# Kernel optimization log

Hardware: AMD Instinct MI355X
Metric: run time of the kernel (lower is better)

The kernel has to match this reference:

```python
import jax, jax.numpy as jnp
import numpy as np

N_NODES = 100000
N_EDGES = 1600000
IN_DIM, HIDDEN, OUT = 128, 64, 32


def setup_inputs() -> dict:
    key = jax.random.key(0)
    k1, k2, k3, k4 = jax.random.split(key, 4)
    x = jax.random.normal(k1, (N_NODES, IN_DIM), dtype=jnp.float32)
    edge_index = jax.random.randint(k2, (2, N_EDGES), 0, N_NODES, dtype=jnp.int64)
    # Glorot-style init for GCN weights
    W1 = jax.random.normal(k3, (IN_DIM, HIDDEN), dtype=jnp.float32) / np.sqrt(IN_DIM)
    b1 = jnp.zeros((HIDDEN,), dtype=jnp.float32)
    W2 = jax.random.normal(k4, (HIDDEN, OUT), dtype=jnp.float32) / np.sqrt(HIDDEN)
    b2 = jnp.zeros((OUT,), dtype=jnp.float32)
    return {"x": x, "edge_index": edge_index, "W1": W1, "b1": b1, "W2": W2, "b2": b2}


def _gcn_conv(x, src, dst, W, b, n_nodes):
    """PyG GCNConv: h = W x; symmetric-normalized scatter-add over edges
    (self-loops already appended to src/dst)."""
    h = x @ W  # [N, F_out] — transform first (F_out <= F_in)
    ones = jnp.ones_like(dst, dtype=h.dtype)
    deg = jax.ops.segment_sum(ones, dst, num_segments=n_nodes)  # in-degree incl. self-loop
    dinv = jnp.where(deg > 0, jax.lax.rsqrt(deg), 0.0)
    norm = dinv[src] * dinv[dst]  # [E]
    msg = h[src] * norm[:, None]  # [E, F_out] — dominant gather
    agg = jax.ops.segment_sum(msg, dst, num_segments=n_nodes)  # [N, F_out]
    return agg + b


def reference(x, edge_index, W1, b1, W2, b2):
    n_nodes = x.shape[0]
    loops = jnp.arange(n_nodes, dtype=edge_index.dtype)
    src = jnp.concatenate([edge_index[0], loops])
    dst = jnp.concatenate([edge_index[1], loops])
    h = jax.nn.relu(_gcn_conv(x, src, dst, W1, b1, n_nodes))
    out = jax.nn.relu(_gcn_conv(h, src, dst, W2, b2, n_nodes))
    return out
```

## Files before the change

kernel.cpp:

```cpp
#include <hip/hip_runtime.h>

#define IN_DIM 128
#define HID    64
#define OUTD   32

#define BSHIFT 9
#define BNODES 512
#define NB     196
#define BCAP   16384
#define CHUNK  4096

#define XPAD   136

typedef __attribute__((ext_vector_type(8))) short bf16x8;
typedef __attribute__((ext_vector_type(4))) float f32x4;


__device__ __forceinline__ unsigned bfp2(float x, float y) {
    unsigned a = __float_as_uint(x); a = a + 0x7FFF + ((a >> 16) & 1);
    unsigned b = __float_as_uint(y); b = b + 0x7FFF + ((b >> 16) & 1);
    return (a >> 16) | (b & 0xFFFF0000u);
}

__device__ __forceinline__ unsigned short bf1(float x) {
    unsigned u = __float_as_uint(x);
    u += 0x7FFF + ((u >> 16) & 1);
    return (unsigned short)(u >> 16);
}

__device__ __forceinline__ void acc8(float* f, uint4 q) {
    f[0] += __uint_as_float(q.x << 16); f[1] += __uint_as_float(q.x & 0xFFFF0000u);
    f[2] += __uint_as_float(q.y << 16); f[3] += __uint_as_float(q.y & 0xFFFF0000u);
    f[4] += __uint_as_float(q.z << 16); f[5] += __uint_as_float(q.z & 0xFFFF0000u);
    f[6] += __uint_as_float(q.w << 16); f[7] += __uint_as_float(q.w & 0xFFFF0000u);
}


__global__ void k_binit(int* __restrict__ bucketCursor) {
    int t = threadIdx.x;
    if (t < NB) bucketCursor[t] = t * BCAP;
}


__launch_bounds__(256)
__global__ void k_bscatter(const int* __restrict__ src, const int* __restrict__ dst,
                           int* __restrict__ bucketCursor, int* __restrict__ ebuf, int E) {
    __shared__ int h[NB];
    __shared__ int lbase[NB];
    __shared__ int lcur[NB];
    int t = threadIdx.x;
    int base = blockIdx.x * CHUNK;
    int end = min(base + CHUNK, E);
    for (int i = t; i < NB; i += 256) { h[i] = 0; lcur[i] = 0; }
    __syncthreads();
    for (int i = base + t; i < end; i += 256)
        atomicAdd(&h[dst[i] >> BSHIFT], 1);
    __syncthreads();
    for (int i = t; i < NB; i += 256)
        lbase[i] = h[i] ? atomicAdd(&bucketCursor[i], h[i]) : 0;
    __syncthreads();
    for (int i = base + t; i < end; i += 256) {
        int d = dst[i];
        int b = d >> BSHIFT;
        int off = atomicAdd(&lcur[b], 1);
        ebuf[lbase[b] + off] = (src[i] << BSHIFT) | (d & (BNODES - 1));
    }
}


__launch_bounds__(256)
__global__ void k_bfinal(const int* __restrict__ ebuf, const int* __restrict__ bucketCursor,
                         int* __restrict__ rs, int* __restrict__ re, float* __restrict__ dinv,
                         int* __restrict__ csr, int N) {
    __shared__ int hist[BNODES];
    __shared__ int rsl[BNODES];
    __shared__ int ssum[256];
    int t = threadIdx.x;
    int b = blockIdx.x;
    int nodeBase = b << BSHIFT;
    int ebase = b * BCAP;
    int eend = bucketCursor[b];

    hist[t] = 0; hist[t + 256] = 0;
    __syncthreads();
    for (int i = ebase + t; i < eend; i += 256)
        atomicAdd(&hist[__builtin_nontemporal_load(ebuf + i) & (BNODES - 1)], 1);
    __syncthreads();

    int h0 = hist[2 * t], h1 = hist[2 * t + 1];
    ssum[t] = h0 + h1;
    __syncthreads();
    for (int off = 1; off < 256; off <<= 1) {
        int u = (t >= off) ? ssum[t - off] : 0;
        __syncthreads();
        ssum[t] += u;
        __syncthreads();
    }
    int excl = ssum[t] - h0 - h1;
    rsl[2 * t]     = excl;
    rsl[2 * t + 1] = excl + h0;

    int n0 = nodeBase + 2 * t, n1 = n0 + 1;
    if (n0 < N) {
        rs[n0] = ebase + excl;           re[n0] = ebase + excl + h0;
        dinv[n0] = rsqrtf((float)h0 + 1.0f);
    }
    if (n1 < N) {
        rs[n1] = ebase + excl + h0;      re[n1] = ebase + excl + h0 + h1;
        dinv[n1] = rsqrtf((float)h1 + 1.0f);
    }

    hist[2 * t] = 0; hist[2 * t + 1] = 0;
    __syncthreads();

    for (int i = ebase + t; i < eend; i += 256) {
        int p = ebuf[i];
        int l = p & (BNODES - 1);
        int off = atomicAdd(&hist[l], 1);
        csr[ebase + rsl[l] + off] = ((unsigned)p) >> BSHIFT;
    }
}


__launch_bounds__(256)
__global__ void k_gemm1(const float* __restrict__ x, const float* __restrict__ W1,
                        const float* __restrict__ dinv, unsigned short* __restrict__ hs1b, int N) {
    __shared__ unsigned short xsb[64 * XPAD];
    __shared__ unsigned short wsb[64 * XPAD];
    const int t = threadIdx.x;
    const int base = blockIdx.x * 64;

    for (int i = t; i < IN_DIM * HID; i += 256) {
        int k = i >> 6, n = i & 63;
        wsb[n * XPAD + k] = bf1(W1[i]);
    }
    {
        const float4* s4 = (const float4*)(x + (size_t)base * IN_DIM);
        #pragma unroll
        for (int j = 0; j < 8; ++j) {
            int idx = t + j * 256;
            int r = idx >> 5, k4 = (idx & 31) * 4;
            ushort4 o;
            if (base + r < N) {
                float4 v = s4[idx];
                o.x = bf1(v.x); o.y = bf1(v.y); o.z = bf1(v.z); o.w = bf1(v.w);
            } else {
                o.x = 0; o.y = 0; o.z = 0; o.w = 0;
            }
            *(ushort4*)&xsb[r * XPAD + k4] = o;
        }
    }
    __syncthreads();

    const int lane = t & 63;
    const int w    = t >> 6;
    const int lr   = lane & 15;
    const int kg   = lane >> 4;

    f32x4 acc0 = {0,0,0,0}, acc1 = {0,0,0,0}, acc2 = {0,0,0,0}, acc3 = {0,0,0,0};
    #pragma unroll
    for (int kb = 0; kb < 4; ++kb) {
        int ko = kb * 32 + kg * 8;
        bf16x8 af = *(const bf16x8*)&xsb[(w * 16 + lr) * XPAD + ko];
        bf16x8 b0 = *(const bf16x8*)&wsb[( 0 + lr) * XPAD + ko];
        bf16x8 b1 = *(const bf16x8*)&wsb[(16 + lr) * XPAD + ko];
        bf16x8 b2 = *(const bf16x8*)&wsb[(32 + lr) * XPAD + ko];
        bf16x8 b3 = *(const bf16x8*)&wsb[(48 + lr) * XPAD + ko];
        acc0 = __builtin_amdgcn_mfma_f32_16x16x32_bf16(af, b0, acc0, 0, 0, 0);
        acc1 = __builtin_amdgcn_mfma_f32_16x16x32_bf16(af, b1, acc1, 0, 0, 0);
        acc2 = __builtin_amdgcn_mfma_f32_16x16x32_bf16(af, b2, acc2, 0, 0, 0);
        acc3 = __builtin_amdgcn_mfma_f32_16x16x32_bf16(af, b3, acc3, 0, 0, 0);
    }

    #pragma unroll
    for (int j = 0; j < 4; ++j) {
        int node = base + w * 16 + kg * 4 + j;
        if (node < N) {
            float d = dinv[node];
            unsigned short* o = hs1b + (size_t)node * HID + lr;
            o[0]  = bf1(acc0[j] * d);
            o[16] = bf1(acc1[j] * d);
            o[32] = bf1(acc2[j] * d);
            o[48] = bf1(acc3[j] * d);
        }
    }
}


__launch_bounds__(256)
__global__ void k_fuse2(const uint4* __restrict__ hs, const int* __restrict__ rs,
                        const int* __restrict__ re, const int* __restrict__ csr,
                        const float* __restrict__ dinv,
                        const float* __restrict__ b1, const float* __restrict__ W2,
                        uint2* __restrict__ hs2b, int N) {
    __shared__ float Ws[HID * OUTD];
    __shared__ float L1s[32 * 68];
    const int t = threadIdx.x;
    const int base = blockIdx.x * 32;

    for (int i = t; i < HID * OUTD / 4; i += 256)
        ((float4*)Ws)[i] = ((const float4*)W2)[i];

    {
        int node = base + (t >> 3);
        int lane = t & 7;
        float fa[8] = {0,0,0,0,0,0,0,0};
        float fb[8] = {0,0,0,0,0,0,0,0};
        float fc[8] = {0,0,0,0,0,0,0,0};
        float fd[8] = {0,0,0,0,0,0,0,0};
        if (node < N) {
            acc8(fa, hs[(size_t)node * 8 + lane]);
            int i = rs[node], end = re[node];
            for (; i + 4 <= end; i += 4) {
                int s0 = __builtin_nontemporal_load(csr + i);
                int s1 = __builtin_nontemporal_load(csr + i + 1);
                int s2 = __builtin_nontemporal_load(csr + i + 2);
                int s3 = __builtin_nontemporal_load(csr + i + 3);
                uint4 q0 = hs[(size_t)s0 * 8 + lane];
                uint4 q1 = hs[(size_t)s1 * 8 + lane];
                uint4 q2 = hs[(size_t)s2 * 8 + lane];
                uint4 q3 = hs[(size_t)s3 * 8 + lane];
                acc8(fa, q0); acc8(fb, q1); acc8(fc, q2); acc8(fd, q3);
            }
            if (i + 2 <= end) {
                int s0 = __builtin_nontemporal_load(csr + i);
                int s1 = __builtin_nontemporal_load(csr + i + 1);
                uint4 q0 = hs[(size_t)s0 * 8 + lane];
                uint4 q1 = hs[(size_t)s1 * 8 + lane];
                acc8(fa, q0); acc8(fb, q1);
                i += 2;
            }
            if (i < end) {
                int s0 = __builtin_nontemporal_load(csr + i);
                acc8(fa, hs[(size_t)s0 * 8 + lane]);
            }
            float dn = dinv[node];
            const float4* bb4 = (const float4*)(b1 + lane * 8);
            float4 bv0 = bb4[0], bv1 = bb4[1];
            float* Lrow = &L1s[(t >> 3) * 68 + lane * 8];
            Lrow[0] = fmaxf((fa[0] + fb[0] + fc[0] + fd[0]) * dn + bv0.x, 0.0f);
            Lrow[1] = fmaxf((fa[1] + fb[1] + fc[1] + fd[1]) * dn + bv0.y, 0.0f);
            Lrow[2] = fmaxf((fa[2] + fb[2] + fc[2] + fd[2]) * dn + bv0.z, 0.0f);
            Lrow[3] = fmaxf((fa[3] + fb[3] + fc[3] + fd[3]) * dn + bv0.w, 0.0f);
            Lrow[4] = fmaxf((fa[4] + fb[4] + fc[4] + fd[4]) * dn + bv1.x, 0.0f);
            Lrow[5] = fmaxf((fa[5] + fb[5] + fc[5] + fd[5]) * dn + bv1.y, 0.0f);
            Lrow[6] = fmaxf((fa[6] + fb[6] + fc[6] + fd[6]) * dn + bv1.z, 0.0f);
            Lrow[7] = fmaxf((fa[7] + fb[7] + fc[7] + fd[7]) * dn + bv1.w, 0.0f);
        } else {
            float* Lrow = &L1s[(t >> 3) * 68 + lane * 8];
            #pragma unroll
            for (int j = 0; j < 8; ++j) Lrow[j] = 0.0f;
        }
    }
    __syncthreads();

    {
        const int fq = t & 7;
        const int nl = t >> 3;
        float4 a = {0,0,0,0};
        #pragma unroll 8
        for (int k = 0; k < HID; ++k) {
            float4 w = ((const float4*)Ws)[k * 8 + fq];
            float xv = L1s[nl * 68 + k];
            a.x += xv * w.x; a.y += xv * w.y; a.z += xv * w.z; a.w += xv * w.w;
        }
        int n = base + nl;
        if (n < N) {
            float d = dinv[n];
            a.x *= d; a.y *= d; a.z *= d; a.w *= d;
            hs2b[(size_t)n * 8 + fq] = make_uint2(bfp2(a.x, a.y), bfp2(a.z, a.w));
        }
    }
}


__launch_bounds__(256)
__global__ void k_agg2(const uint4* __restrict__ hs, const int* __restrict__ rs,
                       const int* __restrict__ re, const int* __restrict__ csr,
                       const float* __restrict__ dinv,
                       const float* __restrict__ b2, float* __restrict__ out, int N) {
    int tid = blockIdx.x * 256 + threadIdx.x;
    int node = tid >> 2;
    if (node >= N) return;
    int lane = tid & 3;

    float fa[8] = {0,0,0,0,0,0,0,0};
    float fb[8] = {0,0,0,0,0,0,0,0};
    float fc[8] = {0,0,0,0,0,0,0,0};
    float fd[8] = {0,0,0,0,0,0,0,0};
    acc8(fa, hs[(size_t)node * 4 + lane]);
    int i = rs[node], end = re[node];
    for (; i + 4 <= end; i += 4) {
        int s0 = __builtin_nontemporal_load(csr + i);
        int s1 = __builtin_nontemporal_load(csr + i + 1);
        int s2 = __builtin_nontemporal_load(csr + i + 2);
        int s3 = __builtin_nontemporal_load(csr + i + 3);
        uint4 q0 = hs[(size_t)s0 * 4 + lane];
        uint4 q1 = hs[(size_t)s1 * 4 + lane];
        uint4 q2 = hs[(size_t)s2 * 4 + lane];
        uint4 q3 = hs[(size_t)s3 * 4 + lane];
        acc8(fa, q0); acc8(fb, q1); acc8(fc, q2); acc8(fd, q3);
    }
    if (i + 2 <= end) {
        int s0 = __builtin_nontemporal_load(csr + i);
        int s1 = __builtin_nontemporal_load(csr + i + 1);
        uint4 q0 = hs[(size_t)s0 * 4 + lane];
        uint4 q1 = hs[(size_t)s1 * 4 + lane];
        acc8(fa, q0); acc8(fb, q1);
        i += 2;
    }
    if (i < end) {
        int s0 = __builtin_nontemporal_load(csr + i);
        acc8(fa, hs[(size_t)s0 * 4 + lane]);
    }
    float dn = dinv[node];
    const float4* bb4 = (const float4*)(b2 + lane * 8);
    float4 b0 = bb4[0], b1v = bb4[1];
    float4 o0, o1;
    o0.x = fmaxf((fa[0] + fb[0] + fc[0] + fd[0]) * dn + b0.x, 0.0f);
    o0.y = fmaxf((fa[1] + fb[1] + fc[1] + fd[1]) * dn + b0.y, 0.0f);
    o0.z = fmaxf((fa[2] + fb[2] + fc[2] + fd[2]) * dn + b0.z, 0.0f);
    o0.w = fmaxf((fa[3] + fb[3] + fc[3] + fd[3]) * dn + b0.w, 0.0f);
    o1.x = fmaxf((fa[4] + fb[4] + fc[4] + fd[4]) * dn + b1v.x, 0.0f);
    o1.y = fmaxf((fa[5] + fb[5] + fc[5] + fd[5]) * dn + b1v.y, 0.0f);
    o1.z = fmaxf((fa[6] + fb[6] + fc[6] + fd[6]) * dn + b1v.z, 0.0f);
    o1.w = fmaxf((fa[7] + fb[7] + fc[7] + fd[7]) * dn + b1v.w, 0.0f);
    float4* o = (float4*)(out + (size_t)node * OUTD + lane * 8);
    o[0] = o0;
    o[1] = o1;
}


extern "C" void kernel_launch(void* const* d_in, const int* in_sizes, int n_in,
                              void* d_out, int out_size, void* d_ws, size_t ws_size,
                              hipStream_t stream) {
    const float* x  = (const float*)d_in[0];
    const int*   ei = (const int*)  d_in[1];
    const float* W1 = (const float*)d_in[2];
    const float* b1 = (const float*)d_in[3];
    const float* W2 = (const float*)d_in[4];
    const float* b2 = (const float*)d_in[5];

    const int N = in_sizes[0] / IN_DIM;
    const int E = in_sizes[1] / 2;
    const int* srcI = ei;
    const int* dstI = ei + E;
    float* out = (float*)d_out;

    float* dinv         = (float*)d_ws;
    int*   rs           = (int*)d_ws + 131072;
    int*   re           = (int*)d_ws + 2 * 131072;
    int*   bucketCursor = (int*)d_ws + 3 * 131072;
    int*   ebuf         = (int*)d_ws + 4 * 131072;
    int*   csr          = ebuf + (size_t)NB * BCAP;
    uint2* hs1b         = (uint2*)(csr + (size_t)NB * BCAP);
    uint2* hs2b         = hs1b + (size_t)N * 16;

    k_binit   <<<1, 256, 0, stream>>>(bucketCursor);
    k_bscatter<<<(E + CHUNK - 1) / CHUNK, 256, 0, stream>>>(srcI, dstI, bucketCursor, ebuf, E);
    k_bfinal  <<<NB, 256, 0, stream>>>(ebuf, bucketCursor, rs, re, dinv, csr, N);

    k_gemm1<<<(N + 63) / 64, 256, 0, stream>>>(x, W1, dinv, (unsigned short*)hs1b, N);
    k_fuse2<<<(N + 31) / 32, 256, 0, stream>>>((const uint4*)hs1b, rs, re, csr, dinv, b1, W2, hs2b, N);
    k_agg2 <<<(N * 4 + 255) / 256, 256, 0, stream>>>((const uint4*)hs2b, rs, re, csr, dinv, b2, out, N);
}
```

Before: 145.7 us.

## Vectorize edge loads in bucketing kernels and software-pipeline CSR index loads in aggregation

```diff
diff --git a/kernel.cpp b/kernel.cpp
--- a/kernel.cpp
+++ b/kernel.cpp
@@ -48,23 +48,43 @@
     __shared__ int h[NB];
     __shared__ int lbase[NB];
     __shared__ int lcur[NB];
-    int t = threadIdx.x;
-    int base = blockIdx.x * CHUNK;
-    int end = min(base + CHUNK, E);
+    const int t = threadIdx.x;
+    const int base = blockIdx.x * CHUNK;
+    const int nI4 = (min(CHUNK, E - base)) >> 2;
+    const int4* d4 = (const int4*)(dst + base);
+    const int4* s4 = (const int4*)(src + base);
+
+    int4 dv0, dv1, dv2, dv3;
+    const bool v0 = t < nI4, v1 = t + 256 < nI4, v2 = t + 512 < nI4, v3 = t + 768 < nI4;
+    if (v0) dv0 = d4[t];
+    if (v1) dv1 = d4[t + 256];
+    if (v2) dv2 = d4[t + 512];
+    if (v3) dv3 = d4[t + 768];
+
     for (int i = t; i < NB; i += 256) { h[i] = 0; lcur[i] = 0; }
     __syncthreads();
-    for (int i = base + t; i < end; i += 256)
-        atomicAdd(&h[dst[i] >> BSHIFT], 1);
-    __syncthreads();
+
+    if (v0) { atomicAdd(&h[dv0.x >> BSHIFT], 1); atomicAdd(&h[dv0.y >> BSHIFT], 1);
+              atomicAdd(&h[dv0.z >> BSHIFT], 1); atomicAdd(&h[dv0.w >> BSHIFT], 1); }
+    if (v1) { atomicAdd(&h[dv1.x >> BSHIFT], 1); atomicAdd(&h[dv1.y >> BSHIFT], 1);
+              atomicAdd(&h[dv1.z >> BSHIFT], 1); atomicAdd(&h[dv1.w >> BSHIFT], 1); }
+    if (v2) { atomicAdd(&h[dv2.x >> BSHIFT], 1); atomicAdd(&h[dv2.y >> BSHIFT], 1);
+              atomicAdd(&h[dv2.z >> BSHIFT], 1); atomicAdd(&h[dv2.w >> BSHIFT], 1); }
+    if (v3) { atomicAdd(&h[dv3.x >> BSHIFT], 1); atomicAdd(&h[dv3.y >> BSHIFT], 1);
+              atomicAdd(&h[dv3.z >> BSHIFT], 1); atomicAdd(&h[dv3.w >> BSHIFT], 1); }
+    __syncthreads();
+
     for (int i = t; i < NB; i += 256)
         lbase[i] = h[i] ? atomicAdd(&bucketCursor[i], h[i]) : 0;
     __syncthreads();
-    for (int i = base + t; i < end; i += 256) {
-        int d = dst[i];
-        int b = d >> BSHIFT;
-        int off = atomicAdd(&lcur[b], 1);
-        ebuf[lbase[b] + off] = (src[i] << BSHIFT) | (d & (BNODES - 1));
-    }
+
+    #define SC1(D, S) { int b_ = (D) >> BSHIFT; int off_ = atomicAdd(&lcur[b_], 1); \
+                        ebuf[lbase[b_] + off_] = ((S) << BSHIFT) | ((D) & (BNODES - 1)); }
+    if (v0) { int4 sv = s4[t];       SC1(dv0.x, sv.x); SC1(dv0.y, sv.y); SC1(dv0.z, sv.z); SC1(dv0.w, sv.w); }
+    if (v1) { int4 sv = s4[t + 256]; SC1(dv1.x, sv.x); SC1(dv1.y, sv.y); SC1(dv1.z, sv.z); SC1(dv1.w, sv.w); }
+    if (v2) { int4 sv = s4[t + 512]; SC1(dv2.x, sv.x); SC1(dv2.y, sv.y); SC1(dv2.z, sv.z); SC1(dv2.w, sv.w); }
+    if (v3) { int4 sv = s4[t + 768]; SC1(dv3.x, sv.x); SC1(dv3.y, sv.y); SC1(dv3.z, sv.z); SC1(dv3.w, sv.w); }
+    #undef SC1
 }
 
 
@@ -75,16 +95,25 @@
     __shared__ int hist[BNODES];
     __shared__ int rsl[BNODES];
     __shared__ int ssum[256];
-    int t = threadIdx.x;
-    int b = blockIdx.x;
-    int nodeBase = b << BSHIFT;
-    int ebase = b * BCAP;
-    int eend = bucketCursor[b];
+    const int t = threadIdx.x;
+    const int b = blockIdx.x;
+    const int nodeBase = b << BSHIFT;
+    const int ebase = b * BCAP;
+    const int cnt = bucketCursor[b] - ebase;
+    const int nI4 = cnt >> 2;
+    const int4* e4 = (const int4*)(ebuf + ebase);
 
     hist[t] = 0; hist[t + 256] = 0;
     __syncthreads();
-    for (int i = ebase + t; i < eend; i += 256)
-        atomicAdd(&hist[__builtin_nontemporal_load(ebuf + i) & (BNODES - 1)], 1);
+    for (int i = t; i < nI4; i += 256) {
+        int4 v = e4[i];
+        atomicAdd(&hist[v.x & (BNODES - 1)], 1);
+        atomicAdd(&hist[v.y & (BNODES - 1)], 1);
+        atomicAdd(&hist[v.z & (BNODES - 1)], 1);
+        atomicAdd(&hist[v.w & (BNODES - 1)], 1);
+    }
+    if (t < (cnt & 3))
+        atomicAdd(&hist[ebuf[ebase + (nI4 << 2) + t] & (BNODES - 1)], 1);
     __syncthreads();
 
     int h0 = hist[2 * t], h1 = hist[2 * t + 1];
@@ -113,12 +142,15 @@
     hist[2 * t] = 0; hist[2 * t + 1] = 0;
     __syncthreads();
 
-    for (int i = ebase + t; i < eend; i += 256) {
-        int p = ebuf[i];
-        int l = p & (BNODES - 1);
-        int off = atomicAdd(&hist[l], 1);
-        csr[ebase + rsl[l] + off] = ((unsigned)p) >> BSHIFT;
-    }
+    #define FILL1(P) { int l_ = (P) & (BNODES - 1); int off_ = atomicAdd(&hist[l_], 1); \
+                       csr[ebase + rsl[l_] + off_] = ((unsigned)(P)) >> BSHIFT; }
+    for (int i = t; i < nI4; i += 256) {
+        int4 v = e4[i];
+        FILL1(v.x); FILL1(v.y); FILL1(v.z); FILL1(v.w);
+    }
+    if (t < (cnt & 3))
+        FILL1(ebuf[ebase + (nI4 << 2) + t]);
+    #undef FILL1
 }
 
 
@@ -211,28 +243,32 @@
         if (node < N) {
             acc8(fa, hs[(size_t)node * 8 + lane]);
             int i = rs[node], end = re[node];
-            for (; i + 4 <= end; i += 4) {
+            int lim = i + ((end - i) & ~3);
+            if (i < lim) {
                 int s0 = __builtin_nontemporal_load(csr + i);
                 int s1 = __builtin_nontemporal_load(csr + i + 1);
                 int s2 = __builtin_nontemporal_load(csr + i + 2);
                 int s3 = __builtin_nontemporal_load(csr + i + 3);
+                for (i += 4; i < lim; i += 4) {
+                    uint4 q0 = hs[(size_t)s0 * 8 + lane];
+                    uint4 q1 = hs[(size_t)s1 * 8 + lane];
+                    uint4 q2 = hs[(size_t)s2 * 8 + lane];
+                    uint4 q3 = hs[(size_t)s3 * 8 + lane];
+                    s0 = __builtin_nontemporal_load(csr + i);
+                    s1 = __builtin_nontemporal_load(csr + i + 1);
+                    s2 = __builtin_nontemporal_load(csr + i + 2);
+                    s3 = __builtin_nontemporal_load(csr + i + 3);
+                    acc8(fa, q0); acc8(fb, q1); acc8(fc, q2); acc8(fd, q3);
+                }
                 uint4 q0 = hs[(size_t)s0 * 8 + lane];
                 uint4 q1 = hs[(size_t)s1 * 8 + lane];
                 uint4 q2 = hs[(size_t)s2 * 8 + lane];
                 uint4 q3 = hs[(size_t)s3 * 8 + lane];
                 acc8(fa, q0); acc8(fb, q1); acc8(fc, q2); acc8(fd, q3);
             }
-            if (i + 2 <= end) {
-                int s0 = __builtin_nontemporal_load(csr + i);
-                int s1 = __builtin_nontemporal_load(csr + i + 1);
-                uint4 q0 = hs[(size_t)s0 * 8 + lane];
-                uint4 q1 = hs[(size_t)s1 * 8 + lane];
-                acc8(fa, q0); acc8(fb, q1);
-                i += 2;
-            }
-            if (i < end) {
-                int s0 = __builtin_nontemporal_load(csr + i);
-                acc8(fa, hs[(size_t)s0 * 8 + lane]);
+            for (; lim < end; ++lim) {
+                int s = __builtin_nontemporal_load(csr + lim);
+                acc8(fa, hs[(size_t)s * 8 + lane]);
             }
             float dn = dinv[node];
             const float4* bb4 = (const float4*)(b1 + lane * 8);
@@ -290,28 +326,32 @@
     float fd[8] = {0,0,0,0,0,0,0,0};
     acc8(fa, hs[(size_t)node * 4 + lane]);
     int i = rs[node], end = re[node];
-    for (; i + 4 <= end; i += 4) {
+    int lim = i + ((end - i) & ~3);
+    if (i < lim) {
         int s0 = __builtin_nontemporal_load(csr + i);
         int s1 = __builtin_nontemporal_load(csr + i + 1);
         int s2 = __builtin_nontemporal_load(csr + i + 2);
         int s3 = __builtin_nontemporal_load(csr + i + 3);
+        for (i += 4; i < lim; i += 4) {
+            uint4 q0 = hs[(size_t)s0 * 4 + lane];
+            uint4 q1 = hs[(size_t)s1 * 4 + lane];
+            uint4 q2 = hs[(size_t)s2 * 4 + lane];
+            uint4 q3 = hs[(size_t)s3 * 4 + lane];
+            s0 = __builtin_nontemporal_load(csr + i);
+            s1 = __builtin_nontemporal_load(csr + i + 1);
+            s2 = __builtin_nontemporal_load(csr + i + 2);
+            s3 = __builtin_nontemporal_load(csr + i + 3);
+            acc8(fa, q0); acc8(fb, q1); acc8(fc, q2); acc8(fd, q3);
+        }
         uint4 q0 = hs[(size_t)s0 * 4 + lane];
         uint4 q1 = hs[(size_t)s1 * 4 + lane];
         uint4 q2 = hs[(size_t)s2 * 4 + lane];
         uint4 q3 = hs[(size_t)s3 * 4 + lane];
         acc8(fa, q0); acc8(fb, q1); acc8(fc, q2); acc8(fd, q3);
     }
-    if (i + 2 <= end) {
-        int s0 = __builtin_nontemporal_load(csr + i);
-        int s1 = __builtin_nontemporal_load(csr + i + 1);
-        uint4 q0 = hs[(size_t)s0 * 4 + lane];
-        uint4 q1 = hs[(size_t)s1 * 4 + lane];
-        acc8(fa, q0); acc8(fb, q1);
-        i += 2;
-    }
-    if (i < end) {
-        int s0 = __builtin_nontemporal_load(csr + i);
-        acc8(fa, hs[(size_t)s0 * 4 + lane]);
+    for (; lim < end; ++lim) {
+        int s = __builtin_nontemporal_load(csr + lim);
+        acc8(fa, hs[(size_t)s * 4 + lane]);
     }
     float dn = dinv[node];
     const float4* bb4 = (const float4*)(b2 + lane * 8);
```

New measurement: 132.0 us. 1.1x faster.
